# Optimization experiments

Measured on AMD Instinct MI355X. Metric: run time of the kernel, lower is better.

## Reference

```python
import jax, jax.numpy as jnp
import numpy as np
from jax import lax

DIM = 1024      # model dim
DS = 16         # d_state
DC = 4          # d_conv
EXP = 2
DI = DIM * EXP  # d_inner = 2048
B, L = 2, 1024


def setup_inputs() -> dict:
    key = jax.random.key(0)
    ks = jax.random.split(key, 10)
    s = lambda k, shape, sc: jax.random.normal(k, shape, jnp.float32) * sc
    return {
        "x": s(ks[0], (B, L, DIM), 1.0),
        "norm_w": jnp.ones((DIM,), jnp.float32),
        "norm_b": jnp.zeros((DIM,), jnp.float32),
        "in_proj_w": s(ks[1], (2 * DI, DIM), DIM ** -0.5),
        "conv_w": s(ks[2], (DI, 1, DC), DC ** -0.5),   # depthwise: (out=DI, in/groups=1, K)
        "conv_b": jnp.zeros((DI,), jnp.float32),
        "x_proj_w": s(ks[3], (2 * DS + 1, DI), DI ** -0.5),
        "dt_w": s(ks[4], (DI, 1), 1.0),
        "dt_b": jax.random.uniform(ks[5], (DI,), jnp.float32, -0.001, 0.001),
        "A_log": s(ks[6], (DI, DS), 1.0),              # self.A (randn); A = -exp(A_log)
        "D_skip": jnp.ones((DI,), jnp.float32),
        "out_proj_w": s(ks[7], (DIM, DI), DI ** -0.5),
    }


def _ssm(x, x_proj_w, dt_w, dt_b, A_log, D_skip):
    # x: (B, L, DI)
    xp = jnp.einsum('bli,pi->blp', x, x_proj_w)            # (B, L, 2*DS+1)
    delta = jax.nn.softplus(xp[..., :1] * dt_w[:, 0] + dt_b)  # (B, L, DI)
    Bp = xp[..., 1:DS + 1]                                  # (B, L, DS)
    Cp = xp[..., DS + 1:]                                   # (B, L, DS)
    A = -jnp.exp(A_log)                                     # (DI, DS)
    dA = jnp.exp(delta[..., None] * A)                      # (B, L, DI, DS)
    dB = delta[..., None] * Bp[:, :, None, :] * x[..., None]  # (B, L, DI, DS)

    def step(h, inp):
        dA_t, dB_t, C_t = inp                               # (B,DI,DS),(B,DI,DS),(B,DS)
        h = dA_t * h + dB_t
        return h, jnp.einsum('bdn,bn->bd', h, C_t)

    h0 = jnp.zeros((x.shape[0], DI, DS), x.dtype)
    _, ys = lax.scan(step, h0, (jnp.swapaxes(dA, 0, 1),
                                jnp.swapaxes(dB, 0, 1),
                                jnp.swapaxes(Cp, 0, 1)))
    y = jnp.swapaxes(ys, 0, 1)                              # (B, L, DI)
    return y + x * D_skip


def reference(x, norm_w, norm_b, in_proj_w, conv_w, conv_b,
              x_proj_w, dt_w, dt_b, A_log, D_skip, out_proj_w):
    # LayerNorm
    mu = x.mean(-1, keepdims=True)
    var = ((x - mu) ** 2).mean(-1, keepdims=True)
    xn = (x - mu) * lax.rsqrt(var + 1e-5) * norm_w + norm_b
    # input projection and gate split
    xz = jnp.einsum('bld,pd->blp', xn, in_proj_w)           # (B, L, 2*DI)
    xi, z = xz[..., :DI], xz[..., DI:]
    # causal depthwise conv (torch pads K-1 both sides then slices [:L] == left-pad K-1)
    xc = lax.conv_general_dilated(jnp.swapaxes(xi, 1, 2), conv_w, (1,),
                                  [(DC - 1, 0)], feature_group_count=DI,
                                  dimension_numbers=('NCH', 'OIH', 'NCH'))
    xc = jnp.swapaxes(xc + conv_b[None, :, None], 1, 2)     # (B, L, DI)
    xc = jax.nn.silu(xc)
    y = _ssm(xc, x_proj_w, dt_w, dt_b, A_log, D_skip)
    y = y * jax.nn.silu(z)
    return x + jnp.einsum('bli,di->bld', y, out_proj_w)
```

## Files before the change

### kernel.cpp

```cpp
#include <hip/hip_runtime.h>
#include <stdint.h>

#define BATCH 2
#define SEQ   1024
#define DIM_  1024
#define DS_   16
#define DI_   2048
#define NTOK  (BATCH*SEQ)
#define NSEG  32
#define LSEG  (SEQ/NSEG)

typedef unsigned short u16;
using s16x8 = __attribute__((ext_vector_type(8))) short;
using f32x4 = __attribute__((ext_vector_type(4))) float;
using u16x4 = __attribute__((ext_vector_type(4))) unsigned short;
using u16x8 = __attribute__((ext_vector_type(8))) unsigned short;

__device__ __forceinline__ float bf2f(u16 u) {
  union { unsigned int i; float f; } c; c.i = ((unsigned int)u) << 16; return c.f;
}
__device__ __forceinline__ u16 f2bf(float f) {
  union { float f; unsigned int i; } c; c.f = f;
  unsigned int r = c.i + 0x7fffu + ((c.i >> 16) & 1u);
  return (u16)(r >> 16);
}
__device__ __forceinline__ float softplus_f(float x) {
  return (x > 15.f) ? x : __logf(1.f + __expf(x));
}

__global__ __launch_bounds__(256) void cvt_pad_kernel(const float* __restrict__ a,
    u16* __restrict__ o) {
  int i = blockIdx.x * 256 + threadIdx.x;
  if (i >= 32768) return;
  int p = (i * 4) >> 11;
  u16x4 r;
  if (p < 33) {
    float4 v = ((const float4*)a)[i];
    r[0] = f2bf(v.x); r[1] = f2bf(v.y); r[2] = f2bf(v.z); r[3] = f2bf(v.w);
  } else {
    r[0] = 0; r[1] = 0; r[2] = 0; r[3] = 0;
  }
  ((u16x4*)o)[i] = r;
}

__global__ __launch_bounds__(256) void ln_kernel(const float* __restrict__ x,
    const float* __restrict__ w, const float* __restrict__ b, u16* __restrict__ xn) {
  int t = blockIdx.x, tid = threadIdx.x;
  const float* row = x + (size_t)t * DIM_;
  float4 v = ((const float4*)row)[tid];
  float f[4] = {v.x, v.y, v.z, v.w};
  float s = 0.f, sq = 0.f;
#pragma unroll
  for (int j = 0; j < 4; j++) { s += f[j]; sq += f[j] * f[j]; }
#pragma unroll
  for (int m = 1; m < 64; m <<= 1) { s += __shfl_xor(s, m); sq += __shfl_xor(sq, m); }
  __shared__ float rs_[4], rq_[4];
  int wv = tid >> 6;
  if ((tid & 63) == 0) { rs_[wv] = s; rq_[wv] = sq; }
  __syncthreads();
  s = rs_[0] + rs_[1] + rs_[2] + rs_[3];
  sq = rq_[0] + rq_[1] + rq_[2] + rq_[3];
  float mu = s * (1.0f / DIM_);
  float var = sq * (1.0f / DIM_) - mu * mu;
  float rstd = rsqrtf(var + 1e-5f);
  float4 wn = ((const float4*)w)[tid];
  float4 bn = ((const float4*)b)[tid];
  u16x4 o;
  o[0] = f2bf((f[0] - mu) * rstd * wn.x + bn.x);
  o[1] = f2bf((f[1] - mu) * rstd * wn.y + bn.y);
  o[2] = f2bf((f[2] - mu) * rstd * wn.z + bn.z);
  o[3] = f2bf((f[3] - mu) * rstd * wn.w + bn.w);
  *(u16x4*)(xn + (size_t)t * DIM_ + tid * 4) = o;
}

template<int TBM, int TBN, int BK, typename OUT, int EPI, int WF32, int KSPLIT = 1>
__global__ __launch_bounds__(256) void gemm_bt(const u16* __restrict__ A,
    const void* __restrict__ Wt_, OUT* __restrict__ C, const float* __restrict__ X,
    int M, int N, int K) {
  constexpr int LDT = BK + 8;
  constexpr int TPR = BK / 8;
  constexpr int RPP = 256 / TPR;
  constexpr int ALn = TBM / RPP;
  constexpr int BLn = TBN / RPP;
  constexpr int KK = BK / 32;
  constexpr int WM = TBM / 2, WN = TBN / 2;
  constexpr int MI = WM / 16, NJ = WN / 16;
  __shared__ __align__(16) u16 sA[TBM * LDT];
  __shared__ __align__(16) u16 sB[TBN * LDT];
  const int tid = threadIdx.x;
  const int lane = tid & 63, wv = tid >> 6;
  const int wm = (wv >> 1) * WM, wn = (wv & 1) * WN;
  const int bm0 = blockIdx.y * TBM, bn0 = blockIdx.x * TBN;
  const int q = lane >> 4, r16 = lane & 15;
  const int srow = tid / TPR, scol = (tid % TPR) * 8;
  const int kc = K / KSPLIT;
  const int k0 = (KSPLIT > 1) ? blockIdx.z * kc : 0;
  const int kend = k0 + kc;

  f32x4 acc[MI][NJ];
#pragma unroll
  for (int i = 0; i < MI; i++)
#pragma unroll
    for (int j = 0; j < NJ; j++)
#pragma unroll
      for (int r = 0; r < 4; r++) acc[i][j][r] = 0.f;

  const u16* Ag = A + (size_t)bm0 * K + scol + k0;
  const u16* Wgh = (const u16*)Wt_ + (size_t)bn0 * K + scol + k0;
  const float* Wgf = (const float*)Wt_ + (size_t)bn0 * K + scol + k0;
  s16x8 ra[ALn], rb[BLn];
  float4 rbf[BLn][2];
#pragma unroll
  for (int i = 0; i < ALn; i++) ra[i] = *(const s16x8*)(Ag + (size_t)(srow + i * RPP) * K);
  if constexpr (WF32) {
#pragma unroll
    for (int i = 0; i < BLn; i++) {
      const float* p = Wgf + (size_t)(srow + i * RPP) * K;
      rbf[i][0] = *(const float4*)p;
      rbf[i][1] = *(const float4*)(p + 4);
    }
  } else {
#pragma unroll
    for (int i = 0; i < BLn; i++) rb[i] = *(const s16x8*)(Wgh + (size_t)(srow + i * RPP) * K);
  }

  for (int kt = k0; kt < kend; kt += BK) {
    __syncthreads();
#pragma unroll
    for (int i = 0; i < ALn; i++) *(s16x8*)&sA[(srow + i * RPP) * LDT + scol] = ra[i];
    if constexpr (WF32) {
#pragma unroll
      for (int i = 0; i < BLn; i++) {
        u16x8 wb;
        wb[0] = f2bf(rbf[i][0].x); wb[1] = f2bf(rbf[i][0].y);
        wb[2] = f2bf(rbf[i][0].z); wb[3] = f2bf(rbf[i][0].w);
        wb[4] = f2bf(rbf[i][1].x); wb[5] = f2bf(rbf[i][1].y);
        wb[6] = f2bf(rbf[i][1].z); wb[7] = f2bf(rbf[i][1].w);
        *(u16x8*)&sB[(srow + i * RPP) * LDT + scol] = wb;
      }
    } else {
#pragma unroll
      for (int i = 0; i < BLn; i++) *(s16x8*)&sB[(srow + i * RPP) * LDT + scol] = rb[i];
    }
    __syncthreads();
    int kn = kt + BK - k0;
    if (kn < kc) {
#pragma unroll
      for (int i = 0; i < ALn; i++) ra[i] = *(const s16x8*)(Ag + (size_t)(srow + i * RPP) * K + kn);
      if constexpr (WF32) {
#pragma unroll
        for (int i = 0; i < BLn; i++) {
          const float* p = Wgf + (size_t)(srow + i * RPP) * K + kn;
          rbf[i][0] = *(const float4*)p;
          rbf[i][1] = *(const float4*)(p + 4);
        }
      } else {
#pragma unroll
        for (int i = 0; i < BLn; i++) rb[i] = *(const s16x8*)(Wgh + (size_t)(srow + i * RPP) * K + kn);
      }
    }
#pragma unroll
    for (int kk = 0; kk < KK; kk++) {
      s16x8 fa[MI], fb[NJ];
#pragma unroll
      for (int i = 0; i < MI; i++)
        fa[i] = *(const s16x8*)&sA[(wm + i * 16 + r16) * LDT + kk * 32 + q * 8];
#pragma unroll
      for (int j = 0; j < NJ; j++)
        fb[j] = *(const s16x8*)&sB[(wn + j * 16 + r16) * LDT + kk * 32 + q * 8];
#pragma unroll
      for (int i = 0; i < MI; i++)
#pragma unroll
        for (int j = 0; j < NJ; j++)
          acc[i][j] = __builtin_amdgcn_mfma_f32_16x16x32_bf16(fa[i], fb[j], acc[i][j], 0, 0, 0);
    }
  }
  OUT* Cz = C + ((KSPLIT > 1) ? (size_t)blockIdx.z * M * N : 0);
#pragma unroll
  for (int i = 0; i < MI; i++)
#pragma unroll
    for (int j = 0; j < NJ; j++) {
      int row0 = bm0 + wm + i * 16 + q * 4;
      int col = bn0 + wn + j * 16 + r16;
#pragma unroll
      for (int r = 0; r < 4; r++) {
        size_t off = (size_t)(row0 + r) * N + col;
        float v = acc[i][j][r];
        if constexpr (EPI == 1) v += X[off];
        if constexpr (sizeof(OUT) == 2) Cz[off] = f2bf(v);
        else                            Cz[off] = v;
      }
    }
}

__global__ __launch_bounds__(256) void reduce_xp_kernel(const float* __restrict__ part,
    float* __restrict__ xp) {
  int g = blockIdx.x * 256 + threadIdx.x;
  constexpr size_t STR = (size_t)NTOK * 64;
  float s = 0.f;
#pragma unroll
  for (int k = 0; k < 8; k++) s += part[(size_t)k * STR + g];
  xp[g] = s;
}

__global__ __launch_bounds__(256) void reduce_out_kernel(const float* __restrict__ part,
    const float* __restrict__ x, float* __restrict__ out) {
  int g = blockIdx.x * 256 + threadIdx.x;
  constexpr size_t STR = (size_t)NTOK * DIM_ / 4;
  float4 a = ((const float4*)part)[g];
  float4 b = ((const float4*)part)[g + STR];
  float4 xv = ((const float4*)x)[g];
  float4 o;
  o.x = xv.x + a.x + b.x;
  o.y = xv.y + a.y + b.y;
  o.z = xv.z + a.z + b.z;
  o.w = xv.w + a.w + b.w;
  ((float4*)out)[g] = o;
}

__global__ __launch_bounds__(256) void conv_silu_kernel(const u16* __restrict__ xz,
    const float* __restrict__ cw, const float* __restrict__ cb, u16* __restrict__ xc) {
  int t = blockIdx.x;
  int l = t & (SEQ - 1);
  int c0 = threadIdx.x * 8;
  float acc[8], wk[8][4];
#pragma unroll
  for (int j = 0; j < 8; j++) {
    float4 wv = ((const float4*)cw)[c0 + j];
    wk[j][0] = wv.x; wk[j][1] = wv.y; wk[j][2] = wv.z; wk[j][3] = wv.w;
    acc[j] = cb[c0 + j];
  }
#pragma unroll
  for (int k = 0; k < 4; k++) {
    int lk = l - 3 + k;
    if (lk >= 0) {
      u16x8 v = *(const u16x8*)(xz + (size_t)(t - 3 + k) * (2 * DI_) + c0);
#pragma unroll
      for (int j = 0; j < 8; j++) acc[j] = fmaf(bf2f(v[j]), wk[j][k], acc[j]);
    }
  }
  u16x8 o;
#pragma unroll
  for (int j = 0; j < 8; j++) {
    float a = acc[j];
    o[j] = f2bf(a / (1.0f + __expf(-a)));
  }
  *(u16x8*)(xc + (size_t)t * DI_ + c0) = o;
}

__global__ __launch_bounds__(256) void delta_bc_kernel(const float* __restrict__ xp,
    const float* __restrict__ dtw, const float* __restrict__ dtb,
    u16* __restrict__ xz, float* __restrict__ bc) {
  int t = blockIdx.x;
  int tid = threadIdx.x;
  int c0 = tid * 8;
  float dr = xp[(size_t)t * 64];
  float wv[8], bv[8];
  *(float4*)wv = ((const float4*)(dtw + c0))[0];
  *(float4*)(wv + 4) = ((const float4*)(dtw + c0))[1];
  *(float4*)bv = ((const float4*)(dtb + c0))[0];
  *(float4*)(bv + 4) = ((const float4*)(dtb + c0))[1];
  u16x8 o;
#pragma unroll
  for (int j = 0; j < 8; j++) o[j] = f2bf(softplus_f(dr * wv[j] + bv[j]));
  *(u16x8*)(xz + (size_t)t * (2 * DI_) + c0) = o;
  if (tid < 32) bc[(size_t)t * 32 + tid] = xp[(size_t)t * 64 + 1 + tid];
}

__global__ __launch_bounds__(256) void scan_pass1(const float* __restrict__ bc,
    const u16* __restrict__ dlt, const u16* __restrict__ xc,
    const float* __restrict__ A_log, float* __restrict__ P, float* __restrict__ Q) {
  int tid = threadIdx.x;
  int lane = tid & 63, wv = tid >> 6;
  int nl = (lane & 3) * 4;
  int d = blockIdx.x * 64 + wv * 16 + (lane >> 2);
  int s = blockIdx.y, b = blockIdx.z;
  int t0 = b * SEQ + s * LSEG;
  float4 Ain = *(const float4*)(A_log + d * DS_ + nl);
  f32x4 Av;
  Av[0] = -__expf(Ain.x); Av[1] = -__expf(Ain.y);
  Av[2] = -__expf(Ain.z); Av[3] = -__expf(Ain.w);
  f32x4 Pv, h;
#pragma unroll
  for (int i = 0; i < 4; i++) { Pv[i] = 1.f; h[i] = 0.f; }
#pragma unroll 4
  for (int j = 0; j < LSEG; j++) {
    int t = t0 + j;
    float delta = bf2f(dlt[(size_t)t * (2 * DI_) + d]);
    float xcv = bf2f(xc[(size_t)t * DI_ + d]);
    float4 B4 = *(const float4*)(bc + (size_t)t * 32 + nl);
    float du = delta * xcv;
#pragma unroll
    for (int i = 0; i < 4; i++) {
      float a = __expf(delta * Av[i]);
      Pv[i] *= a;
      float bi = (i == 0) ? B4.x : (i == 1) ? B4.y : (i == 2) ? B4.z : B4.w;
      h[i] = fmaf(a, h[i], du * bi);
    }
  }
  size_t idx = ((size_t)((b * NSEG + s) * DI_ + d)) * 16 + nl;
  *(f32x4*)(P + idx) = Pv;
  *(f32x4*)(Q + idx) = h;
}

__global__ __launch_bounds__(256) void scan_combine(const float* __restrict__ P,
    float* __restrict__ Q) {
  int g = blockIdx.x * 256 + threadIdx.x;
  int n = g & 15, d = (g >> 4) & (DI_ - 1), b = g >> 15;
  size_t base = ((size_t)b * NSEG * DI_ + d) * 16 + n;
  constexpr size_t STR = (size_t)DI_ * 16;
  float p_[NSEG], q_[NSEG];
#pragma unroll
  for (int s = 0; s < NSEG; s++) {
    p_[s] = P[base + s * STR];
    q_[s] = Q[base + s * STR];
  }
  float hh = 0.f;
#pragma unroll
  for (int s = 0; s < NSEG; s++) {
    Q[base + s * STR] = hh;
    hh = fmaf(p_[s], hh, q_[s]);
  }
}

__global__ __launch_bounds__(256) void scan_pass2(const float* __restrict__ bc,
    const u16* __restrict__ dlt, const u16* __restrict__ xc,
    const float* __restrict__ A_log, const float* __restrict__ Hin,
    u16* __restrict__ yb) {
  int tid = threadIdx.x;
  int lane = tid & 63, wv = tid >> 6;
  int nl = (lane & 3) * 4;
  int d = blockIdx.x * 64 + wv * 16 + (lane >> 2);
  int s = blockIdx.y, b = blockIdx.z;
  int t0 = b * SEQ + s * LSEG;
  float4 Ain = *(const float4*)(A_log + d * DS_ + nl);
  f32x4 Av;
  Av[0] = -__expf(Ain.x); Av[1] = -__expf(Ain.y);
  Av[2] = -__expf(Ain.z); Av[3] = -__expf(Ain.w);
  size_t idx = ((size_t)((b * NSEG + s) * DI_ + d)) * 16 + nl;
  f32x4 h = *(const f32x4*)(Hin + idx);
#pragma unroll 4
  for (int j = 0; j < LSEG; j++) {
    int t = t0 + j;
    float delta = bf2f(dlt[(size_t)t * (2 * DI_) + d]);
    float xcv = bf2f(xc[(size_t)t * DI_ + d]);
    float4 B4 = *(const float4*)(bc + (size_t)t * 32 + nl);
    float4 C4 = *(const float4*)(bc + (size_t)t * 32 + 16 + nl);
    float du = delta * xcv;
#pragma unroll
    for (int i = 0; i < 4; i++) {
      float a = __expf(delta * Av[i]);
      float bi = (i == 0) ? B4.x : (i == 1) ? B4.y : (i == 2) ? B4.z : B4.w;
      h[i] = fmaf(a, h[i], du * bi);
    }
    float p = h[0] * C4.x;
    p = fmaf(h[1], C4.y, p);
    p = fmaf(h[2], C4.z, p);
    p = fmaf(h[3], C4.w, p);
    p += __shfl_xor(p, 1);
    p += __shfl_xor(p, 2);
    if ((lane & 3) == 0) yb[(size_t)t * DI_ + d] = f2bf(p);
  }
}

__global__ __launch_bounds__(256) void gate_kernel(u16* __restrict__ yb,
    const u16* __restrict__ xc, const u16* __restrict__ xz,
    const float* __restrict__ Dskip) {
  int t = blockIdx.x;
  int c0 = threadIdx.x * 8;
  u16x8 pv = *(const u16x8*)(yb + (size_t)t * DI_ + c0);
  u16x8 xcv = *(const u16x8*)(xc + (size_t)t * DI_ + c0);
  u16x8 zv = *(const u16x8*)(xz + (size_t)t * (2 * DI_) + DI_ + c0);
  float Dv[8];
  *(float4*)Dv = ((const float4*)(Dskip + c0))[0];
  *(float4*)(Dv + 4) = ((const float4*)(Dskip + c0))[1];
  u16x8 o;
#pragma unroll
  for (int j = 0; j < 8; j++) {
    float z = bf2f(zv[j]);
    float sz = z / (1.0f + __expf(-z));
    o[j] = f2bf((bf2f(pv[j]) + bf2f(xcv[j]) * Dv[j]) * sz);
  }
  *(u16x8*)(yb + (size_t)t * DI_ + c0) = o;
}

extern "C" void kernel_launch(void* const* d_in, const int* in_sizes, int n_in,
                              void* d_out, int out_size, void* d_ws, size_t ws_size,
                              hipStream_t stream) {
  const float* x      = (const float*)d_in[0];
  const float* norm_w = (const float*)d_in[1];
  const float* norm_b = (const float*)d_in[2];
  const float* in_w   = (const float*)d_in[3];
  const float* conv_w = (const float*)d_in[4];
  const float* conv_b = (const float*)d_in[5];
  const float* xproj_w= (const float*)d_in[6];
  const float* dt_w   = (const float*)d_in[7];
  const float* dt_b   = (const float*)d_in[8];
  const float* A_log  = (const float*)d_in[9];
  const float* D_skip = (const float*)d_in[10];
  const float* out_w  = (const float*)d_in[11];
  float* out = (float*)d_out;

  char* ws = (char*)d_ws;
  size_t off = 0;
  auto alloc = [&](size_t bytes) { void* p = ws + off; off += (bytes + 255) & ~255ULL; return p; };
  u16* xpw_bf = (u16*)alloc((size_t)64 * DI_ * 2);
  u16* xz     = (u16*)alloc((size_t)NTOK * 2 * DI_ * 2);
  u16* xc     = (u16*)alloc((size_t)NTOK * DI_ * 2);
  float* xp   = (float*)alloc((size_t)NTOK * 64 * 4);
  float* bc   = (float*)alloc((size_t)NTOK * 32 * 4);
  char* regionA = (char*)alloc((size_t)BATCH * NSEG * DI_ * 16 * 4);
  float* Q = (float*)alloc((size_t)BATCH * NSEG * DI_ * 16 * 4);
  u16* xn   = (u16*)regionA;
  float* P  = (float*)regionA;
  u16* yb   = (u16*)regionA;
  float* xp_part = Q;
  float* out_part = (float*)xz;

  cvt_pad_kernel<<<128, 256, 0, stream>>>(xproj_w, xpw_bf);
  ln_kernel<<<NTOK, 256, 0, stream>>>(x, norm_w, norm_b, xn);
  gemm_bt<128, 64, 64, u16, 0, 1><<<dim3((2 * DI_) / 64, NTOK / 128), 256, 0, stream>>>(
      xn, in_w, xz, nullptr, NTOK, 2 * DI_, DIM_);
  conv_silu_kernel<<<NTOK, 256, 0, stream>>>(xz, conv_w, conv_b, xc);
  gemm_bt<64, 64, 32, float, 0, 0, 8><<<dim3(1, NTOK / 64, 8), 256, 0, stream>>>(
      xc, xpw_bf, xp_part, nullptr, NTOK, 64, DI_);
  reduce_xp_kernel<<<NTOK * 64 / 256, 256, 0, stream>>>(xp_part, xp);
  delta_bc_kernel<<<NTOK, 256, 0, stream>>>(xp, dt_w, dt_b, xz, bc);
  scan_pass1<<<dim3(DI_ / 64, NSEG, BATCH), 256, 0, stream>>>(bc, xz, xc, A_log, P, Q);
  scan_combine<<<BATCH * DI_ * 16 / 256, 256, 0, stream>>>(P, Q);
  scan_pass2<<<dim3(DI_ / 64, NSEG, BATCH), 256, 0, stream>>>(bc, xz, xc, A_log, Q, yb);
  gate_kernel<<<NTOK, 256, 0, stream>>>(yb, xc, xz, D_skip);
  gemm_bt<64, 64, 64, float, 0, 1, 2><<<dim3(DIM_ / 64, NTOK / 64, 2), 256, 0, stream>>>(
      yb, out_w, out_part, nullptr, NTOK, DIM_, DI_);
  reduce_out_kernel<<<NTOK * DIM_ / 4 / 256, 256, 0, stream>>>(out_part, x, out);
}
```

Before: 238.4 us.

## Fuse xp reduction into delta kernel, gate into scan pass2, swizzle GEMM blocks

Merges the split-K reduction of the x_proj partials into the delta/B/C kernel through shared memory, and folds the D-skip residual and SiLU(z) gating into the scan second pass so it writes the gated output directly. This drops two kernel launches and the extra global round trips for xp and yb. It also adds an optional block-index swizzle along N for the in_proj and out_proj GEMMs to change the order in which blocks touch weight tiles and improve cache locality. Within the scan, the gating is done by one lane in four, which adds scattered 2-byte loads of z.

```diff
diff --git a/kernel.cpp b/kernel.cpp
--- a/kernel.cpp
+++ b/kernel.cpp
@@ -73,7 +73,7 @@
   *(u16x4*)(xn + (size_t)t * DIM_ + tid * 4) = o;
 }
 
-template<int TBM, int TBN, int BK, typename OUT, int EPI, int WF32, int KSPLIT = 1>
+template<int TBM, int TBN, int BK, typename OUT, int EPI, int WF32, int KSPLIT = 1, int SWZ = 0>
 __global__ __launch_bounds__(256) void gemm_bt(const u16* __restrict__ A,
     const void* __restrict__ Wt_, OUT* __restrict__ C, const float* __restrict__ X,
     int M, int N, int K) {
@@ -90,7 +90,9 @@
   const int tid = threadIdx.x;
   const int lane = tid & 63, wv = tid >> 6;
   const int wm = (wv >> 1) * WM, wn = (wv & 1) * WN;
-  const int bm0 = blockIdx.y * TBM, bn0 = blockIdx.x * TBN;
+  const int bxl = SWZ ? ((blockIdx.x & 7) * (gridDim.x >> 3) + (blockIdx.x >> 3))
+                      : blockIdx.x;
+  const int bm0 = blockIdx.y * TBM, bn0 = bxl * TBN;
   const int q = lane >> 4, r16 = lane & 15;
   const int srow = tid / TPR, scol = (tid % TPR) * 8;
   const int kc = K / KSPLIT;
@@ -191,16 +193,6 @@
         else                            Cz[off] = v;
       }
     }
-}
-
-__global__ __launch_bounds__(256) void reduce_xp_kernel(const float* __restrict__ part,
-    float* __restrict__ xp) {
-  int g = blockIdx.x * 256 + threadIdx.x;
-  constexpr size_t STR = (size_t)NTOK * 64;
-  float s = 0.f;
-#pragma unroll
-  for (int k = 0; k < 8; k++) s += part[(size_t)k * STR + g];
-  xp[g] = s;
 }
 
 __global__ __launch_bounds__(256) void reduce_out_kernel(const float* __restrict__ part,
@@ -248,13 +240,23 @@
   *(u16x8*)(xc + (size_t)t * DI_ + c0) = o;
 }
 
-__global__ __launch_bounds__(256) void delta_bc_kernel(const float* __restrict__ xp,
+__global__ __launch_bounds__(256) void xp_finish_kernel(const float* __restrict__ part,
     const float* __restrict__ dtw, const float* __restrict__ dtb,
     u16* __restrict__ xz, float* __restrict__ bc) {
   int t = blockIdx.x;
   int tid = threadIdx.x;
+  __shared__ float xps[64];
+  if (tid < 64) {
+    float s = 0.f;
+#pragma unroll
+    for (int k = 0; k < 8; k++)
+      s += part[(size_t)k * NTOK * 64 + (size_t)t * 64 + tid];
+    xps[tid] = s;
+  }
+  __syncthreads();
+  if (tid < 32) bc[(size_t)t * 32 + tid] = xps[1 + tid];
+  float dr = xps[0];
   int c0 = tid * 8;
-  float dr = xp[(size_t)t * 64];
   float wv[8], bv[8];
   *(float4*)wv = ((const float4*)(dtw + c0))[0];
   *(float4*)(wv + 4) = ((const float4*)(dtw + c0))[1];
@@ -264,7 +266,6 @@
 #pragma unroll
   for (int j = 0; j < 8; j++) o[j] = f2bf(softplus_f(dr * wv[j] + bv[j]));
   *(u16x8*)(xz + (size_t)t * (2 * DI_) + c0) = o;
-  if (tid < 32) bc[(size_t)t * 32 + tid] = xp[(size_t)t * 64 + 1 + tid];
 }
 
 __global__ __launch_bounds__(256) void scan_pass1(const float* __restrict__ bc,
@@ -325,8 +326,8 @@
 
 __global__ __launch_bounds__(256) void scan_pass2(const float* __restrict__ bc,
     const u16* __restrict__ dlt, const u16* __restrict__ xc,
-    const float* __restrict__ A_log, const float* __restrict__ Hin,
-    u16* __restrict__ yb) {
+    const float* __restrict__ A_log, const float* __restrict__ Dskip,
+    const float* __restrict__ Hin, u16* __restrict__ yb) {
   int tid = threadIdx.x;
   int lane = tid & 63, wv = tid >> 6;
   int nl = (lane & 3) * 4;
@@ -337,6 +338,7 @@
   f32x4 Av;
   Av[0] = -__expf(Ain.x); Av[1] = -__expf(Ain.y);
   Av[2] = -__expf(Ain.z); Av[3] = -__expf(Ain.w);
+  float Dv = Dskip[d];
   size_t idx = ((size_t)((b * NSEG + s) * DI_ + d)) * 16 + nl;
   f32x4 h = *(const f32x4*)(Hin + idx);
 #pragma unroll 4
@@ -359,29 +361,12 @@
     p = fmaf(h[3], C4.w, p);
     p += __shfl_xor(p, 1);
     p += __shfl_xor(p, 2);
-    if ((lane & 3) == 0) yb[(size_t)t * DI_ + d] = f2bf(p);
-  }
-}
-
-__global__ __launch_bounds__(256) void gate_kernel(u16* __restrict__ yb,
-    const u16* __restrict__ xc, const u16* __restrict__ xz,
-    const float* __restrict__ Dskip) {
-  int t = blockIdx.x;
-  int c0 = threadIdx.x * 8;
-  u16x8 pv = *(const u16x8*)(yb + (size_t)t * DI_ + c0);
-  u16x8 xcv = *(const u16x8*)(xc + (size_t)t * DI_ + c0);
-  u16x8 zv = *(const u16x8*)(xz + (size_t)t * (2 * DI_) + DI_ + c0);
-  float Dv[8];
-  *(float4*)Dv = ((const float4*)(Dskip + c0))[0];
-  *(float4*)(Dv + 4) = ((const float4*)(Dskip + c0))[1];
-  u16x8 o;
-#pragma unroll
-  for (int j = 0; j < 8; j++) {
-    float z = bf2f(zv[j]);
-    float sz = z / (1.0f + __expf(-z));
-    o[j] = f2bf((bf2f(pv[j]) + bf2f(xcv[j]) * Dv[j]) * sz);
-  }
-  *(u16x8*)(yb + (size_t)t * DI_ + c0) = o;
+    if ((lane & 3) == 0) {
+      float z = bf2f(dlt[(size_t)t * (2 * DI_) + DI_ + d]);
+      float sz = z / (1.0f + __expf(-z));
+      yb[(size_t)t * DI_ + d] = f2bf((p + xcv * Dv) * sz);
+    }
+  }
 }
 
 extern "C" void kernel_launch(void* const* d_in, const int* in_sizes, int n_in,
@@ -407,7 +392,6 @@
   u16* xpw_bf = (u16*)alloc((size_t)64 * DI_ * 2);
   u16* xz     = (u16*)alloc((size_t)NTOK * 2 * DI_ * 2);
   u16* xc     = (u16*)alloc((size_t)NTOK * DI_ * 2);
-  float* xp   = (float*)alloc((size_t)NTOK * 64 * 4);
   float* bc   = (float*)alloc((size_t)NTOK * 32 * 4);
   char* regionA = (char*)alloc((size_t)BATCH * NSEG * DI_ * 16 * 4);
   float* Q = (float*)alloc((size_t)BATCH * NSEG * DI_ * 16 * 4);
@@ -419,18 +403,17 @@
 
   cvt_pad_kernel<<<128, 256, 0, stream>>>(xproj_w, xpw_bf);
   ln_kernel<<<NTOK, 256, 0, stream>>>(x, norm_w, norm_b, xn);
-  gemm_bt<128, 64, 64, u16, 0, 1><<<dim3((2 * DI_) / 64, NTOK / 128), 256, 0, stream>>>(
+  gemm_bt<128, 64, 64, u16, 0, 1, 1, 1><<<dim3((2 * DI_) / 64, NTOK / 128), 256, 0, stream>>>(
       xn, in_w, xz, nullptr, NTOK, 2 * DI_, DIM_);
   conv_silu_kernel<<<NTOK, 256, 0, stream>>>(xz, conv_w, conv_b, xc);
   gemm_bt<64, 64, 32, float, 0, 0, 8><<<dim3(1, NTOK / 64, 8), 256, 0, stream>>>(
       xc, xpw_bf, xp_part, nullptr, NTOK, 64, DI_);
-  reduce_xp_kernel<<<NTOK * 64 / 256, 256, 0, stream>>>(xp_part, xp);
-  delta_bc_kernel<<<NTOK, 256, 0, stream>>>(xp, dt_w, dt_b, xz, bc);
+  xp_finish_kernel<<<NTOK, 256, 0, stream>>>(xp_part, dt_w, dt_b, xz, bc);
   scan_pass1<<<dim3(DI_ / 64, NSEG, BATCH), 256, 0, stream>>>(bc, xz, xc, A_log, P, Q);
   scan_combine<<<BATCH * DI_ * 16 / 256, 256, 0, stream>>>(P, Q);
-  scan_pass2<<<dim3(DI_ / 64, NSEG, BATCH), 256, 0, stream>>>(bc, xz, xc, A_log, Q, yb);
-  gate_kernel<<<NTOK, 256, 0, stream>>>(yb, xc, xz, D_skip);
-  gemm_bt<64, 64, 64, float, 0, 1, 2><<<dim3(DIM_ / 64, NTOK / 64, 2), 256, 0, stream>>>(
+  scan_pass2<<<dim3(DI_ / 64, NSEG, BATCH), 256, 0, stream>>>(bc, xz, xc, A_log, D_skip,
+                                                              Q, yb);
+  gemm_bt<64, 64, 64, float, 0, 1, 2, 1><<<dim3(DIM_ / 64, NTOK / 64, 2), 256, 0, stream>>>(
       yb, out_w, out_part, nullptr, NTOK, DIM_, DI_);
   reduce_out_kernel<<<NTOK * DIM_ / 4 / 256, 256, 0, stream>>>(out_part, x, out);
 }
```

New measurement: 242.2 us. No clear change (+1.6%).
